# Kernel tuning notes

Hardware: AMD Instinct MI355X
Metric: run time of the kernel (lower is better)

Reference implementation:

```python
import jax, jax.numpy as jnp
import numpy as np

B, S, D, H = 2, 2048, 1024, 16
DH = D // H  # 64


def setup_inputs() -> dict:
    key = jax.random.key(0)
    ks = jax.random.split(key, 12)
    std = 1.0 / np.sqrt(D)
    inp = {
        "query": jax.random.normal(ks[0], (B, S, D), jnp.float32),
        "key": jax.random.normal(ks[1], (B, S, D), jnp.float32),
        "value": jax.random.normal(ks[2], (B, S, D), jnp.float32),
        # causal mask: 1.0 where attention is disallowed (j > i)
        "mask": jnp.triu(jnp.ones((S, S), jnp.float32), k=1)[None, None, :, :] * jnp.ones((B, 1, 1, 1), jnp.float32),
        "Wq": jax.random.normal(ks[3], (D, D), jnp.float32) * std,
        "bq": jnp.zeros((D,), jnp.float32),
        "Wk": jax.random.normal(ks[4], (D, D), jnp.float32) * std,
        "bk": jnp.zeros((D,), jnp.float32),
        "Wv": jax.random.normal(ks[5], (D, D), jnp.float32) * std,
        "bv": jnp.zeros((D,), jnp.float32),
        "Wo": jax.random.normal(ks[6], (D, D), jnp.float32) * std,
        "bo": jnp.zeros((D,), jnp.float32),
    }
    return inp


def _split_heads(x):
    b, s, _ = x.shape
    return x.reshape(b, s, H, DH).transpose(0, 2, 1, 3)  # [B,H,S,DH]


def reference(query, key, value, mask, Wq, bq, Wk, bk, Wv, bv, Wo, bo):
    q = _split_heads(query @ Wq + bq)
    k = _split_heads(key @ Wk + bk)
    v = _split_heads(value @ Wv + bv)
    scale = jnp.sqrt(jnp.asarray(DH, jnp.float32))
    scores = jnp.einsum("bhqd,bhkd->bhqk", q, k) / scale
    scores = scores + mask * (-1e9)
    attn = jax.nn.softmax(scores, axis=-1)  # [B,H,S,S]
    out = jnp.einsum("bhqk,bhkd->bhqd", attn, v)
    out = out.transpose(0, 2, 1, 3).reshape(query.shape[0], -1, D)
    out = out @ Wo + bo
    return (out, attn)
```

## Files before the change

kernel.cpp:

```cpp
#include <hip/hip_runtime.h>
#include <hip/hip_bf16.h>

typedef __bf16 bf16;
typedef __bf16 bf16x8 __attribute__((ext_vector_type(8)));
typedef __bf16 bf16x4 __attribute__((ext_vector_type(4)));
typedef float f32x4 __attribute__((ext_vector_type(4)));

#define S_LEN 2048
#define D_MODEL 1024
#define N_HEADS 16
#define D_HEAD 64
#define M_ROWS 4096

__global__ void cvt_f32_bf16(const float* __restrict__ in, bf16* __restrict__ out, int n) {
    int i = (blockIdx.x * blockDim.x + threadIdx.x) * 4;
    int stride = gridDim.x * blockDim.x * 4;
    for (; i < n; i += stride) {
        f32x4 v = *(const f32x4*)(in + i);
        bf16x4 o;
        o[0] = (bf16)v[0]; o[1] = (bf16)v[1]; o[2] = (bf16)v[2]; o[3] = (bf16)v[3];
        *(bf16x4*)(out + i) = o;
    }
}

__global__ void cvtT_f32_bf16(const float* __restrict__ in, bf16* __restrict__ out) {
    __shared__ float t[32][33];
    int k0 = blockIdx.x * 32, n0 = blockIdx.y * 32;
    int lr = threadIdx.x & 31, lc = threadIdx.x >> 5;
#pragma unroll
    for (int p = 0; p < 4; ++p)
        t[lc + p * 8][lr] = in[(size_t)(k0 + lc + p * 8) * D_MODEL + n0 + lr];
    __syncthreads();
#pragma unroll
    for (int p = 0; p < 4; ++p)
        out[(size_t)(n0 + lc + p * 8) * D_MODEL + k0 + lr] = (bf16)t[lr][lc + p * 8];
}

__global__ __launch_bounds__(256) void gemm_bf16(
    const bf16* __restrict__ A, const bf16* __restrict__ Bt,
    const float* __restrict__ bias, bf16* __restrict__ outh,
    float* __restrict__ outf, int mode) {
    const int K = D_MODEL;
    __shared__ bf16 Als[128][80];
    __shared__ bf16 Bls[128][80];
    const int tid = threadIdx.x;
    const int lane = tid & 63, wave = tid >> 6;
    const int wm = wave >> 1, wn = wave & 1;
    const int g = lane >> 4, r16 = lane & 15;
    const int m0 = blockIdx.x * 128, n0 = blockIdx.y * 128;
    const int srow = tid >> 3, scol = (tid & 7) * 8;
    f32x4 acc[4][4] = {};
    for (int kt = 0; kt < K; kt += 64) {
        __syncthreads();
#pragma unroll
        for (int p = 0; p < 4; ++p) {
            int row = p * 32 + srow;
            *(bf16x8*)&Als[row][scol] = *(const bf16x8*)(A + (size_t)(m0 + row) * K + kt + scol);
            *(bf16x8*)&Bls[row][scol] = *(const bf16x8*)(Bt + (size_t)(n0 + row) * K + kt + scol);
        }
        __syncthreads();
#pragma unroll
        for (int kk = 0; kk < 2; ++kk) {
            bf16x8 af[4], bfr[4];
#pragma unroll
            for (int i = 0; i < 4; ++i) af[i] = *(const bf16x8*)&Als[wm * 64 + i * 16 + r16][kk * 32 + g * 8];
#pragma unroll
            for (int j = 0; j < 4; ++j) bfr[j] = *(const bf16x8*)&Bls[wn * 64 + j * 16 + r16][kk * 32 + g * 8];
#pragma unroll
            for (int i = 0; i < 4; ++i)
#pragma unroll
                for (int j = 0; j < 4; ++j)
                    acc[i][j] = __builtin_amdgcn_mfma_f32_16x16x32_bf16(af[i], bfr[j], acc[i][j], 0, 0, 0);
        }
    }
#pragma unroll
    for (int i = 0; i < 4; ++i) {
#pragma unroll
        for (int j = 0; j < 4; ++j) {
            int col = n0 + wn * 64 + j * 16 + r16;
            float bv = bias[col];
#pragma unroll
            for (int r = 0; r < 4; ++r) {
                int row = m0 + wm * 64 + i * 16 + g * 4 + r;
                float v = acc[i][j][r] + bv;
                if (mode == 0) {
                    int b = row >> 11, s = row & (S_LEN - 1);
                    int h = col >> 6, dh = col & 63;
                    outh[(size_t)(((b * N_HEADS + h) * S_LEN) + s) * D_HEAD + dh] = (bf16)v;
                } else {
                    outf[(size_t)row * D_MODEL + col] = v;
                }
            }
        }
    }
}

__global__ __launch_bounds__(256) void attn_bf16(
    const bf16* __restrict__ Qh, const bf16* __restrict__ Kh, const bf16* __restrict__ Vh,
    float* __restrict__ attn, bf16* __restrict__ ctx) {
    const int S = S_LEN, DH = D_HEAD;
    __shared__ bf16 Kls[64][80];
    __shared__ bf16 Vt[64][80];
    __shared__ bf16 Pls[4][16][80];
    const int tid = threadIdx.x;
    const int lane = tid & 63, w = tid >> 6;
    const int g = lane >> 4, r16 = lane & 15;
    const int qt = blockIdx.x, bh = blockIdx.y;
    const int q0 = qt * 64;

    bf16x8 qa[2];
#pragma unroll
    for (int kk = 0; kk < 2; ++kk)
        qa[kk] = *(const bf16x8*)(Qh + (size_t)(bh * S + q0 + w * 16 + r16) * DH + kk * 32 + g * 8);

    float rs[4] = {0.f, 0.f, 0.f, 0.f};
    for (int kt = 0; kt <= qt; ++kt) {
        __syncthreads();
#pragma unroll
        for (int sIt = 0; sIt < 2; ++sIt) {
            int slot = tid + sIt * 256;
            int krow = slot >> 3, c8 = (slot & 7) * 8;
            *(bf16x8*)&Kls[krow][c8] =
                *(const bf16x8*)(Kh + (size_t)(bh * S + kt * 64 + krow) * DH + c8);
        }
        __syncthreads();
#pragma unroll
        for (int n = 0; n < 4; ++n) {
            f32x4 s = {0.f, 0.f, 0.f, 0.f};
#pragma unroll
            for (int kk = 0; kk < 2; ++kk) {
                bf16x8 kb = *(const bf16x8*)&Kls[n * 16 + r16][kk * 32 + g * 8];
                s = __builtin_amdgcn_mfma_f32_16x16x32_bf16(qa[kk], kb, s, 0, 0, 0);
            }
            int col = kt * 64 + n * 16 + r16;
#pragma unroll
            for (int r = 0; r < 4; ++r) {
                int row = q0 + w * 16 + g * 4 + r;
                float p = (col <= row) ? __expf(s[r] * 0.125f) : 0.f;
                rs[r] += p;
            }
        }
    }
#pragma unroll
    for (int r = 0; r < 4; ++r) {
        rs[r] += __shfl_xor(rs[r], 1);
        rs[r] += __shfl_xor(rs[r], 2);
        rs[r] += __shfl_xor(rs[r], 4);
        rs[r] += __shfl_xor(rs[r], 8);
    }
    float inv[4];
#pragma unroll
    for (int r = 0; r < 4; ++r) inv[r] = 1.f / rs[r];

    f32x4 oacc[4] = {};
    for (int kt = 0; kt <= qt; ++kt) {
        __syncthreads();
#pragma unroll
        for (int sIt = 0; sIt < 2; ++sIt) {
            int slot = tid + sIt * 256;
            int krow = slot >> 3, c8 = (slot & 7) * 8;
            *(bf16x8*)&Kls[krow][c8] =
                *(const bf16x8*)(Kh + (size_t)(bh * S + kt * 64 + krow) * DH + c8);
            bf16x8 vv = *(const bf16x8*)(Vh + (size_t)(bh * S + kt * 64 + krow) * DH + c8);
#pragma unroll
            for (int e = 0; e < 8; ++e) Vt[c8 + e][krow] = vv[e];
        }
        __syncthreads();
#pragma unroll
        for (int n = 0; n < 4; ++n) {
            f32x4 s = {0.f, 0.f, 0.f, 0.f};
#pragma unroll
            for (int kk = 0; kk < 2; ++kk) {
                bf16x8 kb = *(const bf16x8*)&Kls[n * 16 + r16][kk * 32 + g * 8];
                s = __builtin_amdgcn_mfma_f32_16x16x32_bf16(qa[kk], kb, s, 0, 0, 0);
            }
            int col = kt * 64 + n * 16 + r16;
#pragma unroll
            for (int r = 0; r < 4; ++r) {
                int row = q0 + w * 16 + g * 4 + r;
                float p = (col <= row) ? __expf(s[r] * 0.125f) : 0.f;
                attn[(size_t)(bh * S + row) * S + col] = p * inv[r];
                Pls[w][g * 4 + r][n * 16 + r16] = (bf16)p;
            }
        }
#pragma unroll
        for (int d = 0; d < 4; ++d) {
#pragma unroll
            for (int kk = 0; kk < 2; ++kk) {
                bf16x8 pa = *(const bf16x8*)&Pls[w][r16][kk * 32 + g * 8];
                bf16x8 vb = *(const bf16x8*)&Vt[d * 16 + r16][kk * 32 + g * 8];
                oacc[d] = __builtin_amdgcn_mfma_f32_16x16x32_bf16(pa, vb, oacc[d], 0, 0, 0);
            }
        }
    }
    const int b = bh >> 4, h = bh & 15;
#pragma unroll
    for (int d = 0; d < 4; ++d) {
#pragma unroll
        for (int r = 0; r < 4; ++r) {
            int srowg = q0 + w * 16 + g * 4 + r;
            ctx[(size_t)(b * S + srowg) * D_MODEL + h * D_HEAD + d * 16 + r16] =
                (bf16)(oacc[d][r] * inv[r]);
        }
    }
    int zstart = (qt + 1) * 64;
    for (int rr = 0; rr < 64; ++rr) {
        float* dst = attn + (size_t)(bh * S + q0 + rr) * S;
        for (int c = zstart + tid * 4; c < S; c += 1024) {
            f32x4 z = {0.f, 0.f, 0.f, 0.f};
            *(f32x4*)(dst + c) = z;
        }
    }
}

extern "C" void kernel_launch(void* const* d_in, const int* in_sizes, int n_in,
                              void* d_out, int out_size, void* d_ws, size_t ws_size,
                              hipStream_t stream) {
    const float* query = (const float*)d_in[0];
    const float* key   = (const float*)d_in[1];
    const float* value = (const float*)d_in[2];
    const float* Wq = (const float*)d_in[4];
    const float* bq = (const float*)d_in[5];
    const float* Wk = (const float*)d_in[6];
    const float* bk = (const float*)d_in[7];
    const float* Wv = (const float*)d_in[8];
    const float* bv = (const float*)d_in[9];
    const float* Wo = (const float*)d_in[10];
    const float* bo = (const float*)d_in[11];

    float* out  = (float*)d_out;
    float* attn = out + (size_t)M_ROWS * D_MODEL;

    bf16* ws  = (bf16*)d_ws;
    const size_t MD = (size_t)M_ROWS * D_MODEL;
    const size_t DD = (size_t)D_MODEL * D_MODEL;
    bf16* Xq  = ws;
    bf16* Xk  = Xq + MD;
    bf16* Xv  = Xk + MD;
    bf16* WqT = Xv + MD;
    bf16* WkT = WqT + DD;
    bf16* WvT = WkT + DD;
    bf16* WoT = WvT + DD;
    bf16* Qh  = WoT + DD;
    bf16* Kh  = Qh + MD;
    bf16* Vh  = Kh + MD;
    bf16* Ctx = Vh + MD;

    int n = (int)MD;
    cvt_f32_bf16<<<2048, 256, 0, stream>>>(query, Xq, n);
    cvt_f32_bf16<<<2048, 256, 0, stream>>>(key, Xk, n);
    cvt_f32_bf16<<<2048, 256, 0, stream>>>(value, Xv, n);
    dim3 tg(32, 32);
    cvtT_f32_bf16<<<tg, 256, 0, stream>>>(Wq, WqT);
    cvtT_f32_bf16<<<tg, 256, 0, stream>>>(Wk, WkT);
    cvtT_f32_bf16<<<tg, 256, 0, stream>>>(Wv, WvT);
    cvtT_f32_bf16<<<tg, 256, 0, stream>>>(Wo, WoT);

    dim3 gg(M_ROWS / 128, D_MODEL / 128);
    gemm_bf16<<<gg, 256, 0, stream>>>(Xq, WqT, bq, Qh, nullptr, 0);
    gemm_bf16<<<gg, 256, 0, stream>>>(Xk, WkT, bk, Kh, nullptr, 0);
    gemm_bf16<<<gg, 256, 0, stream>>>(Xv, WvT, bv, Vh, nullptr, 0);

    dim3 ag(S_LEN / 64, 2 * N_HEADS);
    attn_bf16<<<ag, 256, 0, stream>>>(Qh, Kh, Vh, attn, Ctx);

    gemm_bf16<<<gg, 256, 0, stream>>>(Ctx, WoT, bo, nullptr, out, 1);
}
```

Measured before the change: 872.5 us.

## Fuse attention into single pass with pre-transposed V and balanced causal tile order

```diff
diff --git a/kernel.cpp b/kernel.cpp
--- a/kernel.cpp
+++ b/kernel.cpp
@@ -87,25 +87,34 @@
                     int b = row >> 11, s = row & (S_LEN - 1);
                     int h = col >> 6, dh = col & 63;
                     outh[(size_t)(((b * N_HEADS + h) * S_LEN) + s) * D_HEAD + dh] = (bf16)v;
+                } else if (mode == 1) {
+                    outf[(size_t)row * D_MODEL + col] = v;
                 } else {
-                    outf[(size_t)row * D_MODEL + col] = v;
+                    int b = row >> 11, s = row & (S_LEN - 1);
+                    int h = col >> 6, dh = col & 63;
+                    outh[(((size_t)(b * N_HEADS + h)) * D_HEAD + dh) * S_LEN + s] = (bf16)v;
                 }
             }
         }
     }
 }
 
-__global__ __launch_bounds__(256) void attn_bf16(
-    const bf16* __restrict__ Qh, const bf16* __restrict__ Kh, const bf16* __restrict__ Vh,
+__global__ __launch_bounds__(256) void attn_fused(
+    const bf16* __restrict__ Qh, const bf16* __restrict__ Kh, const bf16* __restrict__ VT,
     float* __restrict__ attn, bf16* __restrict__ ctx) {
     const int S = S_LEN, DH = D_HEAD;
     __shared__ bf16 Kls[64][80];
-    __shared__ bf16 Vt[64][80];
+    __shared__ bf16 Vls[64][80];
     __shared__ bf16 Pls[4][16][80];
+    __shared__ float rowinv[64];
     const int tid = threadIdx.x;
     const int lane = tid & 63, w = tid >> 6;
     const int g = lane >> 4, r16 = lane & 15;
-    const int qt = blockIdx.x, bh = blockIdx.y;
+    const int id = blockIdx.x;
+    const int bh = id & 31;
+    const int qx = id >> 5;
+    const int a = qx & 7, kq = qx >> 3;
+    const int qt = (kq == 0) ? (31 - a) : (kq == 1) ? (16 + a) : (kq == 2) ? (15 - a) : a;
     const int q0 = qt * 64;
 
     bf16x8 qa[2];
@@ -114,14 +123,17 @@
         qa[kk] = *(const bf16x8*)(Qh + (size_t)(bh * S + q0 + w * 16 + r16) * DH + kk * 32 + g * 8);
 
     float rs[4] = {0.f, 0.f, 0.f, 0.f};
+    f32x4 oacc[4] = {};
     for (int kt = 0; kt <= qt; ++kt) {
         __syncthreads();
 #pragma unroll
         for (int sIt = 0; sIt < 2; ++sIt) {
             int slot = tid + sIt * 256;
-            int krow = slot >> 3, c8 = (slot & 7) * 8;
-            *(bf16x8*)&Kls[krow][c8] =
-                *(const bf16x8*)(Kh + (size_t)(bh * S + kt * 64 + krow) * DH + c8);
+            int srow = slot >> 3, c8 = (slot & 7) * 8;
+            *(bf16x8*)&Kls[srow][c8] =
+                *(const bf16x8*)(Kh + (size_t)(bh * S + kt * 64 + srow) * DH + c8);
+            *(bf16x8*)&Vls[srow][c8] =
+                *(const bf16x8*)(VT + ((size_t)bh * DH + srow) * S + kt * 64 + c8);
         }
         __syncthreads();
 #pragma unroll
@@ -138,6 +150,17 @@
                 int row = q0 + w * 16 + g * 4 + r;
                 float p = (col <= row) ? __expf(s[r] * 0.125f) : 0.f;
                 rs[r] += p;
+                attn[(size_t)(bh * S + row) * S + col] = p;
+                Pls[w][g * 4 + r][n * 16 + r16] = (bf16)p;
+            }
+        }
+#pragma unroll
+        for (int d = 0; d < 4; ++d) {
+#pragma unroll
+            for (int kk = 0; kk < 2; ++kk) {
+                bf16x8 pa = *(const bf16x8*)&Pls[w][r16][kk * 32 + g * 8];
+                bf16x8 vb = *(const bf16x8*)&Vls[d * 16 + r16][kk * 32 + g * 8];
+                oacc[d] = __builtin_amdgcn_mfma_f32_16x16x32_bf16(pa, vb, oacc[d], 0, 0, 0);
             }
         }
     }
@@ -151,47 +174,9 @@
     float inv[4];
 #pragma unroll
     for (int r = 0; r < 4; ++r) inv[r] = 1.f / rs[r];
-
-    f32x4 oacc[4] = {};
-    for (int kt = 0; kt <= qt; ++kt) {
-        __syncthreads();
-#pragma unroll
-        for (int sIt = 0; sIt < 2; ++sIt) {
-            int slot = tid + sIt * 256;
-            int krow = slot >> 3, c8 = (slot & 7) * 8;
-            *(bf16x8*)&Kls[krow][c8] =
-                *(const bf16x8*)(Kh + (size_t)(bh * S + kt * 64 + krow) * DH + c8);
-            bf16x8 vv = *(const bf16x8*)(Vh + (size_t)(bh * S + kt * 64 + krow) * DH + c8);
-#pragma unroll
-            for (int e = 0; e < 8; ++e) Vt[c8 + e][krow] = vv[e];
-        }
-        __syncthreads();
-#pragma unroll
-        for (int n = 0; n < 4; ++n) {
-            f32x4 s = {0.f, 0.f, 0.f, 0.f};
-#pragma unroll
-            for (int kk = 0; kk < 2; ++kk) {
-                bf16x8 kb = *(const bf16x8*)&Kls[n * 16 + r16][kk * 32 + g * 8];
-                s = __builtin_amdgcn_mfma_f32_16x16x32_bf16(qa[kk], kb, s, 0, 0, 0);
-            }
-            int col = kt * 64 + n * 16 + r16;
-#pragma unroll
-            for (int r = 0; r < 4; ++r) {
-                int row = q0 + w * 16 + g * 4 + r;
-                float p = (col <= row) ? __expf(s[r] * 0.125f) : 0.f;
-                attn[(size_t)(bh * S + row) * S + col] = p * inv[r];
-                Pls[w][g * 4 + r][n * 16 + r16] = (bf16)p;
-            }
-        }
-#pragma unroll
-        for (int d = 0; d < 4; ++d) {
-#pragma unroll
-            for (int kk = 0; kk < 2; ++kk) {
-                bf16x8 pa = *(const bf16x8*)&Pls[w][r16][kk * 32 + g * 8];
-                bf16x8 vb = *(const bf16x8*)&Vt[d * 16 + r16][kk * 32 + g * 8];
-                oacc[d] = __builtin_amdgcn_mfma_f32_16x16x32_bf16(pa, vb, oacc[d], 0, 0, 0);
-            }
-        }
+    if (r16 == 0) {
+#pragma unroll
+        for (int r = 0; r < 4; ++r) rowinv[w * 16 + g * 4 + r] = inv[r];
     }
     const int b = bh >> 4, h = bh & 15;
 #pragma unroll
@@ -203,12 +188,26 @@
                 (bf16)(oacc[d][r] * inv[r]);
         }
     }
-    int zstart = (qt + 1) * 64;
-    for (int rr = 0; rr < 64; ++rr) {
-        float* dst = attn + (size_t)(bh * S + q0 + rr) * S;
-        for (int c = zstart + tid * 4; c < S; c += 1024) {
-            f32x4 z = {0.f, 0.f, 0.f, 0.f};
-            *(f32x4*)(dst + c) = z;
+    __syncthreads();
+    {
+        int rr = tid >> 2, q4 = (tid & 3) * 4;
+        int row = q0 + rr;
+        float sc = rowinv[rr];
+        float* prow = attn + (size_t)(bh * S + row) * S;
+        int limit = row + 1;
+        for (int c = q4; c < S; c += 16) {
+            if (c + 4 <= limit) {
+                f32x4 v = *(f32x4*)(prow + c);
+                v *= sc;
+                *(f32x4*)(prow + c) = v;
+            } else if (c >= limit) {
+                f32x4 z = {0.f, 0.f, 0.f, 0.f};
+                *(f32x4*)(prow + c) = z;
+            } else {
+#pragma unroll
+                for (int e = 0; e < 4; ++e)
+                    prow[c + e] = (c + e < limit) ? prow[c + e] * sc : 0.f;
+            }
         }
     }
 }
@@ -243,8 +242,8 @@
     bf16* WoT = WvT + DD;
     bf16* Qh  = WoT + DD;
     bf16* Kh  = Qh + MD;
-    bf16* Vh  = Kh + MD;
-    bf16* Ctx = Vh + MD;
+    bf16* VT  = Kh + MD;
+    bf16* Ctx = VT + MD;
 
     int n = (int)MD;
     cvt_f32_bf16<<<2048, 256, 0, stream>>>(query, Xq, n);
@@ -259,10 +258,9 @@
     dim3 gg(M_ROWS / 128, D_MODEL / 128);
     gemm_bf16<<<gg, 256, 0, stream>>>(Xq, WqT, bq, Qh, nullptr, 0);
     gemm_bf16<<<gg, 256, 0, stream>>>(Xk, WkT, bk, Kh, nullptr, 0);
-    gemm_bf16<<<gg, 256, 0, stream>>>(Xv, WvT, bv, Vh, nullptr, 0);
-
-    dim3 ag(S_LEN / 64, 2 * N_HEADS);
-    attn_bf16<<<ag, 256, 0, stream>>>(Qh, Kh, Vh, attn, Ctx);
+    gemm_bf16<<<gg, 256, 0, stream>>>(Xv, WvT, bv, VT, nullptr, 2);
+
+    attn_fused<<<1024, 256, 0, stream>>>(Qh, Kh, VT, attn, Ctx);
 
     gemm_bf16<<<gg, 256, 0, stream>>>(Ctx, WoT, bo, nullptr, out, 1);
 }
```

Result: slower. 946.1 us (+8.4%).
